# Kernel tuning notes

Measured on AMD Instinct MI355X. Metric: run time of the kernel, lower is better.

The kernel has to match this reference:

```python
import jax, jax.numpy as jnp
import numpy as np

B, N, C, F = 8, 3, 64, 128
H = W = 128


def _up2(x):
    # nearest-neighbor upsample by 2 on the last two axes
    return jnp.repeat(jnp.repeat(x, 2, axis=-2), 2, axis=-1)


def setup_inputs() -> dict:
    key = jax.random.key(0)
    ks = jax.random.split(key, 12)
    s = lambda k, shp, fan: jax.random.normal(k, shp, jnp.float32) * (1.0 / np.sqrt(fan))
    return {
        "contexts": jax.random.normal(ks[0], (B, N, C, H, W), jnp.float32),
        "mainstream": jax.random.normal(ks[1], (B, F, H // 2, W // 2), jnp.float32),
        "Wc": s(ks[2], (C, C), C),        # W_context 1x1 conv weight [out,in]
        "bc": jnp.zeros((C,), jnp.float32),
        "Wf": s(ks[3], (C, F), F),        # W_feat 1x1
        "bf": jnp.zeros((C,), jnp.float32),
        "Wk": s(ks[4], (C, F), F),        # W_key_feat 1x1
        "bk": jnp.zeros((C,), jnp.float32),
        "Vw": s(ks[5], (C, F, 3, 3), F * 9),  # values_conv 3x3, OIHW
        "Vb": jnp.zeros((C,), jnp.float32),
    }


def reference(contexts, mainstream, Wc, bc, Wf, bf, Wk, bk, Vw, Vb):
    # contexts: [B,N,C,H,W], mainstream: [B,F,h,w]
    bias = lambda b: b[None, :, None, None]
    queries = jnp.einsum('bfhw,cf->bchw', mainstream, Wf) + bias(bf)       # [B,C,h,w]
    keys_m = jnp.einsum('bfhw,cf->bchw', mainstream, Wk) + bias(bk)        # [B,C,h,w]
    values = jax.lax.conv_general_dilated(
        mainstream, Vw, (1, 1), 'SAME',
        dimension_numbers=('NCHW', 'OIHW', 'NCHW')) + bias(Vb)             # [B,C,h,w]

    # stack contexts with upsampled mainstream keys, project with W_context (1x1)
    keys_stack = jnp.concatenate([contexts, _up2(keys_m)[:, None]], axis=1)  # [B,N+1,C,H,W]
    keys_proj = jnp.einsum('bnchw,dc->bndhw', keys_stack, Wc) + bc[None, None, :, None, None]

    q_up = _up2(queries)                                                    # [B,C,H,W]
    logits = jnp.einsum('bnchw,bchw->bnhw', keys_proj, q_up)                # [B,N+1,H,W]
    attn = jax.nn.softmax(logits, axis=1)                                   # softmax over contexts

    vals_stack = jnp.concatenate([contexts, _up2(values)[:, None]], axis=1) # [B,N+1,C,H,W]
    out = jnp.einsum('bnchw,bnhw->bchw', vals_stack, attn)                  # [B,C,H,W]
    return out
```

## Files before the change

### kernel.cpp

```cpp
#include <hip/hip_runtime.h>
#include <math.h>

#define CH   64
#define FD   128
#define HS   64
#define FS   128
#define NB   8
#define NCTX 3

#define WS_BQ   4227072
#define WS_AVH  4227136
#define WS_AQH  4264000
#define WS_AQL  4268096
#define WS_AKH  4272192
#define WS_AKL  4276288

typedef short  s16x8  __attribute__((ext_vector_type(8)));
typedef float  f32x16 __attribute__((ext_vector_type(16)));

__device__ inline unsigned short bf16_rne(float x) {
  unsigned u = __float_as_uint(x);
  u += 0x7FFFu + ((u >> 16) & 1u);
  return (unsigned short)(u >> 16);
}
__device__ inline void split2(float x, unsigned short& h, unsigned short& l) {
  h = bf16_rne(x);
  l = bf16_rne(x - __uint_as_float((unsigned)h << 16));
}

__global__ __launch_bounds__(256) void afrag_prep(
    const float* __restrict__ Wc, const float* __restrict__ Wf,
    const float* __restrict__ bf, const float* __restrict__ Wk,
    const float* __restrict__ Vw, float* __restrict__ ws) {
  int id = blockIdx.x * 256 + threadIdx.x;
  unsigned short* avh = (unsigned short*)(ws + WS_AVH);
  unsigned short* aqh = (unsigned short*)(ws + WS_AQH);
  unsigned short* aql = (unsigned short*)(ws + WS_AQL);
  unsigned short* akh = (unsigned short*)(ws + WS_AKH);
  unsigned short* akl = (unsigned short*)(ws + WS_AKL);

  if (id < 9216) {
    int tile = id / 4608, rem = id % 4608;
    int q = rem >> 6, l = rem & 63;
    int am = l & 31, kh = l >> 5;
    int c = tile * 32 + am, tap = q >> 3, kf = q & 7;
#pragma unroll
    for (int j = 0; j < 8; ++j) {
      int f = kf * 16 + kh * 8 + j;
      avh[id * 8 + j] = bf16_rne(Vw[(c * FD + f) * 9 + tap]);
    }
  } else if (id < 10240) {
    int i2 = id - 9216;
    int tile = i2 >> 9, rem = i2 & 511;
    int q = rem >> 6, l = rem & 63;
    int am = l & 31, kh = l >> 5;
    int c = tile * 32 + am;
#pragma unroll
    for (int j = 0; j < 8; ++j) {
      int f = q * 16 + kh * 8 + j;
      float acc = 0.f;
      for (int d = 0; d < CH; ++d)
        acc = fmaf(Wc[d * CH + c], Wf[d * FD + f], acc);
      unsigned short h, lo; split2(acc, h, lo);
      aqh[i2 * 8 + j] = h; aql[i2 * 8 + j] = lo;
    }
  } else if (id < 11264) {
    int i3 = id - 10240;
    int tile = i3 >> 9, rem = i3 & 511;
    int q = rem >> 6, l = rem & 63;
    int am = l & 31, kh = l >> 5;
    int c = tile * 32 + am;
#pragma unroll
    for (int j = 0; j < 8; ++j) {
      int f = q * 16 + kh * 8 + j;
      unsigned short h, lo; split2(Wk[c * FD + f], h, lo);
      akh[i3 * 8 + j] = h; akl[i3 * 8 + j] = lo;
    }
  } else if (id < 11328) {
    int c = id - 11264;
    float acc = 0.f;
    for (int d = 0; d < CH; ++d) acc = fmaf(Wc[d * CH + c], bf[d], acc);
    ws[WS_BQ + c] = acc;
  }
}

__global__ __launch_bounds__(512) void fused_kernel(
    const float* __restrict__ m, const float* __restrict__ Vb,
    const float* __restrict__ bk, const float* __restrict__ ctx,
    float* __restrict__ out, const float* __restrict__ ws) {
  const int b = blockIdx.x >> 6, y = blockIdx.x & 63;
  const int t = threadIdx.x, lane = t & 63;
  const int wave = __builtin_amdgcn_readfirstlane(t >> 6);
  const int am = lane & 31, kh = lane >> 5;

  __shared__ __align__(16) union {
    short HI[3][8][66][2][8];
    struct {
      float  QT[CH * HS];
      float  VAL[CH * HS];
      float4 wpart[2][4][3][16];
      float  L3row[HS];
    } p;
  } U;
  __shared__ float l3red[2][64];

  if (t < 96) {
    int row = t / 32, kf = (t >> 2) & 7, khh = (t >> 1) & 1, col = (t & 1) * 65;
    s16x8 z;
#pragma unroll
    for (int j = 0; j < 8; ++j) z[j] = 0;
    *(s16x8*)&U.HI[row][kf][col][khh][0] = z;
  }

#pragma unroll
  for (int i = 0; i < 6; ++i) {
    const int tk = wave * 6 + i;
    const int row = tk >> 4, kf = (tk >> 1) & 7, khh = tk & 1;
    const int yy = y + row - 1;
    s16x8 hi;
    if (yy >= 0 && yy < HS) {
#pragma unroll
      for (int j = 0; j < 8; ++j) {
        const int f = kf * 16 + khh * 8 + j;
        hi[j] = (short)bf16_rne(m[((b * FD + f) * HS + yy) * HS + lane]);
      }
    } else {
#pragma unroll
      for (int j = 0; j < 8; ++j) hi[j] = 0;
    }
    *(s16x8*)&U.HI[row][kf][lane + 1][khh][0] = hi;
  }
  __syncthreads();

  const int ct = (wave >> 1) & 1;
  const int xh = wave & 1;
  const int x0 = xh * 32, ch0 = ct * 32;

  f32x16 acc, q1, q2, k1, k2;
  float l3part = 0.f;

  if (wave < 4) {
    const unsigned short* avh = (const unsigned short*)(ws + WS_AVH);
#pragma unroll
    for (int i = 0; i < 16; ++i) acc[i] = 0.f;
#pragma unroll 8
    for (int q = 0; q < 72; ++q) {
      const int tap = q >> 3, kf = q & 7;
      const s16x8 ah = *(const s16x8*)(avh + ((ct * 72 + q) * 64 + lane) * 8);
      const s16x8 bh = *(const s16x8*)&U.HI[tap / 3][kf][x0 + am + tap % 3][kh][0];
      acc = __builtin_amdgcn_mfma_f32_32x32x16_bf16(ah, bh, acc, 0, 0, 0);
    }
  } else {
    const unsigned short* aqh = (const unsigned short*)(ws + WS_AQH);
    const unsigned short* aql = (const unsigned short*)(ws + WS_AQL);
    const unsigned short* akh = (const unsigned short*)(ws + WS_AKH);
    const unsigned short* akl = (const unsigned short*)(ws + WS_AKL);
#pragma unroll
    for (int i = 0; i < 16; ++i) { q1[i] = 0.f; q2[i] = 0.f; k1[i] = 0.f; k2[i] = 0.f; }
#pragma unroll
    for (int q = 0; q < 8; ++q) {
      const s16x8 bh = *(const s16x8*)&U.HI[1][q][x0 + am + 1][kh][0];
      s16x8 bl;
#pragma unroll
      for (int j = 0; j < 8; ++j) {
        const float mv = m[((b * FD + q * 16 + kh * 8 + j) * HS + y) * HS + x0 + am];
        const float hf = __uint_as_float(((unsigned)(unsigned short)bh[j]) << 16);
        bl[j] = (short)bf16_rne(mv - hf);
      }
      const s16x8 ah = *(const s16x8*)(aqh + ((ct * 8 + q) * 64 + lane) * 8);
      const s16x8 al = *(const s16x8*)(aql + ((ct * 8 + q) * 64 + lane) * 8);
      const s16x8 kah = *(const s16x8*)(akh + ((ct * 8 + q) * 64 + lane) * 8);
      const s16x8 kal = *(const s16x8*)(akl + ((ct * 8 + q) * 64 + lane) * 8);
      q1 = __builtin_amdgcn_mfma_f32_32x32x16_bf16(ah, bh, q1, 0, 0, 0);
      q1 = __builtin_amdgcn_mfma_f32_32x32x16_bf16(al, bh, q1, 0, 0, 0);
      q2 = __builtin_amdgcn_mfma_f32_32x32x16_bf16(ah, bl, q2, 0, 0, 0);
      k1 = __builtin_amdgcn_mfma_f32_32x32x16_bf16(kah, bh, k1, 0, 0, 0);
      k1 = __builtin_amdgcn_mfma_f32_32x32x16_bf16(kal, bh, k1, 0, 0, 0);
      k2 = __builtin_amdgcn_mfma_f32_32x32x16_bf16(kah, bl, k2, 0, 0, 0);
    }
  }
  __syncthreads();

  if (wave < 4) {
#pragma unroll
    for (int r = 0; r < 16; ++r) {
      const int c = ch0 + (r & 3) + 8 * (r >> 2) + 4 * kh;
      U.p.VAL[c * HS + x0 + am] = acc[r] + Vb[c];
    }
  } else {
#pragma unroll
    for (int r = 0; r < 16; ++r) {
      const int c = ch0 + (r & 3) + 8 * (r >> 2) + 4 * kh;
      const float qvv = q1[r] + q2[r] + ws[WS_BQ + c];
      const float kvv = k1[r] + k2[r] + bk[c];
      U.p.QT[c * HS + x0 + am] = qvv;
      l3part = fmaf(qvv, kvv, l3part);
    }
    if (ct == 1) l3red[xh][lane] = l3part;
  }
  __syncthreads();

  if (wave == 4 || wave == 5) {
    float s = l3part + l3red[xh][lane];
    s += __shfl_xor(s, 32, 64);
    if (kh == 0) U.p.L3row[x0 + am] = s;
  }
  __syncthreads();

  const int u    = t >> 8;
  const int tt   = t & 255;
  const int quad = tt & 15;
  const int cg   = tt >> 4;
  const int wv   = tt >> 6;
  const int c0   = cg * 4;
  const int hrow = 2 * y + u;
  const int cs = FS * FS, ns = CH * FS * FS;

  float* op = out + (size_t)(b * CH) * FS * FS + (size_t)hrow * FS;
  const float* cb = ctx + (size_t)(b * NCTX * CH) * cs + (size_t)hrow * FS;

#pragma unroll 1
  for (int x2 = 0; x2 < 2; ++x2) {
    const int x = x2 * 64 + quad * 4;
    const int w2 = x >> 1;

    float4 cv[3][4];
    float2 qv[4];
#pragma unroll
    for (int j = 0; j < 4; ++j) {
      const int c = c0 + j;
      cv[0][j] = *(const float4*)(cb + x + c * cs);
      cv[1][j] = *(const float4*)(cb + x + ns + c * cs);
      cv[2][j] = *(const float4*)(cb + x + 2 * ns + c * cs);
      qv[j] = *(const float2*)&U.p.QT[c * HS + w2];
    }

    float4 pl[3];
#pragma unroll
    for (int n = 0; n < 3; ++n) {
      pl[n].x = pl[n].y = pl[n].z = pl[n].w = 0.f;
#pragma unroll
      for (int j = 0; j < 4; ++j) {
        pl[n].x = fmaf(cv[n][j].x, qv[j].x, pl[n].x);
        pl[n].y = fmaf(cv[n][j].y, qv[j].x, pl[n].y);
        pl[n].z = fmaf(cv[n][j].z, qv[j].y, pl[n].z);
        pl[n].w = fmaf(cv[n][j].w, qv[j].y, pl[n].w);
      }
    }

#pragma unroll
    for (int n = 0; n < 3; ++n) {
      pl[n].x += __shfl_xor(pl[n].x, 16, 64);
      pl[n].y += __shfl_xor(pl[n].y, 16, 64);
      pl[n].z += __shfl_xor(pl[n].z, 16, 64);
      pl[n].w += __shfl_xor(pl[n].w, 16, 64);
      pl[n].x += __shfl_xor(pl[n].x, 32, 64);
      pl[n].y += __shfl_xor(pl[n].y, 32, 64);
      pl[n].z += __shfl_xor(pl[n].z, 32, 64);
      pl[n].w += __shfl_xor(pl[n].w, 32, 64);
    }
    __syncthreads();
    if ((lane >> 4) == 0) {
#pragma unroll
      for (int n = 0; n < 3; ++n) U.p.wpart[u][wv][n][quad] = pl[n];
    }
    __syncthreads();

    float4 L[3];
#pragma unroll
    for (int n = 0; n < 3; ++n) {
      const float4 p0 = U.p.wpart[u][0][n][quad];
      const float4 p1 = U.p.wpart[u][1][n][quad];
      const float4 p2 = U.p.wpart[u][2][n][quad];
      const float4 p3 = U.p.wpart[u][3][n][quad];
      L[n].x = (p0.x + p1.x) + (p2.x + p3.x);
      L[n].y = (p0.y + p1.y) + (p2.y + p3.y);
      L[n].z = (p0.z + p1.z) + (p2.z + p3.z);
      L[n].w = (p0.w + p1.w) + (p2.w + p3.w);
    }
    const float2 l3v = *(const float2*)&U.p.L3row[w2];

    float A0[4], A1[4], A2[4], A3[4];
    const float* L0p = (const float*)&L[0];
    const float* L1p = (const float*)&L[1];
    const float* L2p = (const float*)&L[2];
#pragma unroll
    for (int k = 0; k < 4; ++k) {
      float L0 = L0p[k], L1 = L1p[k], L2 = L2p[k];
      float L3 = (k < 2) ? l3v.x : l3v.y;
      float mx = fmaxf(fmaxf(L0, L1), fmaxf(L2, L3));
      float e0 = __expf(L0 - mx), e1 = __expf(L1 - mx);
      float e2 = __expf(L2 - mx), e3 = __expf(L3 - mx);
      float inv = 1.f / (e0 + e1 + e2 + e3);
      A0[k] = e0 * inv; A1[k] = e1 * inv; A2[k] = e2 * inv; A3[k] = e3 * inv;
    }

#pragma unroll
    for (int j = 0; j < 4; ++j) {
      const int c = c0 + j;
      const float2 vv = *(const float2*)&U.p.VAL[c * HS + w2];
      float4 o;
      o.x = fmaf(A0[0], cv[0][j].x, fmaf(A1[0], cv[1][j].x, fmaf(A2[0], cv[2][j].x, A3[0] * vv.x)));
      o.y = fmaf(A0[1], cv[0][j].y, fmaf(A1[1], cv[1][j].y, fmaf(A2[1], cv[2][j].y, A3[1] * vv.x)));
      o.z = fmaf(A0[2], cv[0][j].z, fmaf(A1[2], cv[1][j].z, fmaf(A2[2], cv[2][j].z, A3[2] * vv.y)));
      o.w = fmaf(A0[3], cv[0][j].w, fmaf(A1[3], cv[1][j].w, fmaf(A2[3], cv[2][j].w, A3[3] * vv.y)));
      *(float4*)(op + x + c * cs) = o;
    }
  }
}

extern "C" void kernel_launch(void* const* d_in, const int* in_sizes, int n_in,
                              void* d_out, int out_size, void* d_ws, size_t ws_size,
                              hipStream_t stream) {
  const float* ctx = (const float*)d_in[0];
  const float* ms  = (const float*)d_in[1];
  const float* Wc  = (const float*)d_in[2];
  const float* Wf  = (const float*)d_in[4];
  const float* bf  = (const float*)d_in[5];
  const float* Wk  = (const float*)d_in[6];
  const float* bk  = (const float*)d_in[7];
  const float* Vw  = (const float*)d_in[8];
  const float* Vb  = (const float*)d_in[9];
  float* ws  = (float*)d_ws;
  float* out = (float*)d_out;

  afrag_prep<<<45, 256, 0, stream>>>(Wc, Wf, bf, Wk, Vw, ws);
  fused_kernel<<<NB * HS, 512, 0, stream>>>(ms, Vb, bk, ctx, out, ws);
}
```

Baseline: 244.9 us.

## Split each row block into two half-width blocks of 256 threads

The fused kernel now launches twice as many blocks, each handling half the 64-wide mainstream row (32 columns plus halo) with 256 threads instead of 512. Each block builds a smaller bf16 tile, runs one value-conv wave pair and one query/key wave pair, and loops over the two upsampled output rows instead of two x halves. Query/value fragments are hoisted out of that loop, and the L3 reduction is folded directly into register reads, which removes one barrier. The goal is more blocks for better CU occupancy and load balance on the memory-bound context streaming, at the cost of redundant halo loads of the mainstream input.

```diff
diff --git a/kernel.cpp b/kernel.cpp
--- a/kernel.cpp
+++ b/kernel.cpp
@@ -84,62 +84,56 @@
   }
 }
 
-__global__ __launch_bounds__(512) void fused_kernel(
+__global__ __launch_bounds__(256) void fused_kernel(
     const float* __restrict__ m, const float* __restrict__ Vb,
     const float* __restrict__ bk, const float* __restrict__ ctx,
     float* __restrict__ out, const float* __restrict__ ws) {
-  const int b = blockIdx.x >> 6, y = blockIdx.x & 63;
+  const int b  = blockIdx.x >> 7;
+  const int y  = (blockIdx.x >> 1) & 63;
+  const int xh = blockIdx.x & 1;
   const int t = threadIdx.x, lane = t & 63;
   const int wave = __builtin_amdgcn_readfirstlane(t >> 6);
   const int am = lane & 31, kh = lane >> 5;
 
   __shared__ __align__(16) union {
-    short HI[3][8][66][2][8];
+    short HI[3][8][34][2][8];
     struct {
-      float  QT[CH * HS];
-      float  VAL[CH * HS];
-      float4 wpart[2][4][3][16];
-      float  L3row[HS];
+      float  QT[CH][34];
+      float  VAL[CH][34];
+      float4 wpart[4][3][16];
+      float  l3red[2][64];
     } p;
   } U;
-  __shared__ float l3red[2][64];
-
-  if (t < 96) {
-    int row = t / 32, kf = (t >> 2) & 7, khh = (t >> 1) & 1, col = (t & 1) * 65;
-    s16x8 z;
-#pragma unroll
-    for (int j = 0; j < 8; ++j) z[j] = 0;
-    *(s16x8*)&U.HI[row][kf][col][khh][0] = z;
-  }
-
-#pragma unroll
-  for (int i = 0; i < 6; ++i) {
-    const int tk = wave * 6 + i;
+
+  const int gx0 = 32 * xh - 1;
+#pragma unroll
+  for (int i = 0; i < 12; ++i) {
+    const int tk = wave * 12 + i;
     const int row = tk >> 4, kf = (tk >> 1) & 7, khh = tk & 1;
     const int yy = y + row - 1;
-    s16x8 hi;
-    if (yy >= 0 && yy < HS) {
-#pragma unroll
-      for (int j = 0; j < 8; ++j) {
-        const int f = kf * 16 + khh * 8 + j;
-        hi[j] = (short)bf16_rne(m[((b * FD + f) * HS + yy) * HS + lane]);
+    const int gx = gx0 + lane;
+    if (lane < 34) {
+      s16x8 hi;
+      if (yy >= 0 && yy < HS && gx >= 0 && gx < HS) {
+#pragma unroll
+        for (int j = 0; j < 8; ++j) {
+          const int f = kf * 16 + khh * 8 + j;
+          hi[j] = (short)bf16_rne(m[((b * FD + f) * HS + yy) * HS + gx]);
+        }
+      } else {
+#pragma unroll
+        for (int j = 0; j < 8; ++j) hi[j] = 0;
       }
-    } else {
-#pragma unroll
-      for (int j = 0; j < 8; ++j) hi[j] = 0;
-    }
-    *(s16x8*)&U.HI[row][kf][lane + 1][khh][0] = hi;
+      *(s16x8*)&U.HI[row][kf][lane][khh][0] = hi;
+    }
   }
   __syncthreads();
 
-  const int ct = (wave >> 1) & 1;
-  const int xh = wave & 1;
-  const int x0 = xh * 32, ch0 = ct * 32;
-
+  const int ct = wave & 1;
   f32x16 acc, q1, q2, k1, k2;
   float l3part = 0.f;
 
-  if (wave < 4) {
+  if (wave < 2) {
     const unsigned short* avh = (const unsigned short*)(ws + WS_AVH);
 #pragma unroll
     for (int i = 0; i < 16; ++i) acc[i] = 0.f;
@@ -147,7 +141,7 @@
     for (int q = 0; q < 72; ++q) {
       const int tap = q >> 3, kf = q & 7;
       const s16x8 ah = *(const s16x8*)(avh + ((ct * 72 + q) * 64 + lane) * 8);
-      const s16x8 bh = *(const s16x8*)&U.HI[tap / 3][kf][x0 + am + tap % 3][kh][0];
+      const s16x8 bh = *(const s16x8*)&U.HI[tap / 3][kf][am + tap % 3][kh][0];
       acc = __builtin_amdgcn_mfma_f32_32x32x16_bf16(ah, bh, acc, 0, 0, 0);
     }
   } else {
@@ -159,11 +153,11 @@
     for (int i = 0; i < 16; ++i) { q1[i] = 0.f; q2[i] = 0.f; k1[i] = 0.f; k2[i] = 0.f; }
 #pragma unroll
     for (int q = 0; q < 8; ++q) {
-      const s16x8 bh = *(const s16x8*)&U.HI[1][q][x0 + am + 1][kh][0];
+      const s16x8 bh = *(const s16x8*)&U.HI[1][q][am + 1][kh][0];
       s16x8 bl;
 #pragma unroll
       for (int j = 0; j < 8; ++j) {
-        const float mv = m[((b * FD + q * 16 + kh * 8 + j) * HS + y) * HS + x0 + am];
+        const float mv = m[((b * FD + q * 16 + kh * 8 + j) * HS + y) * HS + 32 * xh + am];
         const float hf = __uint_as_float(((unsigned)(unsigned short)bh[j]) << 16);
         bl[j] = (short)bf16_rne(mv - hf);
       }
@@ -181,58 +175,57 @@
   }
   __syncthreads();
 
-  if (wave < 4) {
+  if (wave < 2) {
 #pragma unroll
     for (int r = 0; r < 16; ++r) {
-      const int c = ch0 + (r & 3) + 8 * (r >> 2) + 4 * kh;
-      U.p.VAL[c * HS + x0 + am] = acc[r] + Vb[c];
+      const int c = ct * 32 + (r & 3) + 8 * (r >> 2) + 4 * kh;
+      U.p.VAL[c][am] = acc[r] + Vb[c];
     }
   } else {
 #pragma unroll
     for (int r = 0; r < 16; ++r) {
-      const int c = ch0 + (r & 3) + 8 * (r >> 2) + 4 * kh;
+      const int c = ct * 32 + (r & 3) + 8 * (r >> 2) + 4 * kh;
       const float qvv = q1[r] + q2[r] + ws[WS_BQ + c];
       const float kvv = k1[r] + k2[r] + bk[c];
-      U.p.QT[c * HS + x0 + am] = qvv;
+      U.p.QT[c][am] = qvv;
       l3part = fmaf(qvv, kvv, l3part);
     }
-    if (ct == 1) l3red[xh][lane] = l3part;
+    U.p.l3red[ct][lane] = l3part;
   }
   __syncthreads();
 
-  if (wave == 4 || wave == 5) {
-    float s = l3part + l3red[xh][lane];
-    s += __shfl_xor(s, 32, 64);
-    if (kh == 0) U.p.L3row[x0 + am] = s;
-  }
-  __syncthreads();
-
-  const int u    = t >> 8;
-  const int tt   = t & 255;
-  const int quad = tt & 15;
-  const int cg   = tt >> 4;
-  const int wv   = tt >> 6;
+  const int quad = t & 15;
+  const int cg   = t >> 4;
   const int c0   = cg * 4;
-  const int hrow = 2 * y + u;
+  const int x    = 64 * xh + quad * 4;
+  const int hx   = quad * 2;
   const int cs = FS * FS, ns = CH * FS * FS;
 
-  float* op = out + (size_t)(b * CH) * FS * FS + (size_t)hrow * FS;
-  const float* cb = ctx + (size_t)(b * NCTX * CH) * cs + (size_t)hrow * FS;
+  const float l3a = U.p.l3red[0][hx]     + U.p.l3red[0][hx + 32]
+                  + U.p.l3red[1][hx]     + U.p.l3red[1][hx + 32];
+  const float l3b = U.p.l3red[0][hx + 1] + U.p.l3red[0][hx + 33]
+                  + U.p.l3red[1][hx + 1] + U.p.l3red[1][hx + 33];
+
+  float2 qv[4], vv[4];
+#pragma unroll
+  for (int j = 0; j < 4; ++j) {
+    qv[j] = *(const float2*)&U.p.QT[c0 + j][hx];
+    vv[j] = *(const float2*)&U.p.VAL[c0 + j][hx];
+  }
 
 #pragma unroll 1
-  for (int x2 = 0; x2 < 2; ++x2) {
-    const int x = x2 * 64 + quad * 4;
-    const int w2 = x >> 1;
+  for (int u = 0; u < 2; ++u) {
+    const int hrow = 2 * y + u;
+    const float* cb = ctx + (size_t)(b * NCTX * CH) * cs + (size_t)hrow * FS + x;
+    float* op = out + (size_t)(b * CH) * cs + (size_t)hrow * FS + x;
 
     float4 cv[3][4];
-    float2 qv[4];
 #pragma unroll
     for (int j = 0; j < 4; ++j) {
       const int c = c0 + j;
-      cv[0][j] = *(const float4*)(cb + x + c * cs);
-      cv[1][j] = *(const float4*)(cb + x + ns + c * cs);
-      cv[2][j] = *(const float4*)(cb + x + 2 * ns + c * cs);
-      qv[j] = *(const float2*)&U.p.QT[c * HS + w2];
+      cv[0][j] = *(const float4*)(cb + c * cs);
+      cv[1][j] = *(const float4*)(cb + ns + c * cs);
+      cv[2][j] = *(const float4*)(cb + 2 * ns + c * cs);
     }
 
     float4 pl[3];
@@ -262,23 +255,22 @@
     __syncthreads();
     if ((lane >> 4) == 0) {
 #pragma unroll
-      for (int n = 0; n < 3; ++n) U.p.wpart[u][wv][n][quad] = pl[n];
+      for (int n = 0; n < 3; ++n) U.p.wpart[wave][n][quad] = pl[n];
     }
     __syncthreads();
 
     float4 L[3];
 #pragma unroll
     for (int n = 0; n < 3; ++n) {
-      const float4 p0 = U.p.wpart[u][0][n][quad];
-      const float4 p1 = U.p.wpart[u][1][n][quad];
-      const float4 p2 = U.p.wpart[u][2][n][quad];
-      const float4 p3 = U.p.wpart[u][3][n][quad];
+      const float4 p0 = U.p.wpart[0][n][quad];
+      const float4 p1 = U.p.wpart[1][n][quad];
+      const float4 p2 = U.p.wpart[2][n][quad];
+      const float4 p3 = U.p.wpart[3][n][quad];
       L[n].x = (p0.x + p1.x) + (p2.x + p3.x);
       L[n].y = (p0.y + p1.y) + (p2.y + p3.y);
       L[n].z = (p0.z + p1.z) + (p2.z + p3.z);
       L[n].w = (p0.w + p1.w) + (p2.w + p3.w);
     }
-    const float2 l3v = *(const float2*)&U.p.L3row[w2];
 
     float A0[4], A1[4], A2[4], A3[4];
     const float* L0p = (const float*)&L[0];
@@ -287,7 +279,7 @@
 #pragma unroll
     for (int k = 0; k < 4; ++k) {
       float L0 = L0p[k], L1 = L1p[k], L2 = L2p[k];
-      float L3 = (k < 2) ? l3v.x : l3v.y;
+      float L3 = (k < 2) ? l3a : l3b;
       float mx = fmaxf(fmaxf(L0, L1), fmaxf(L2, L3));
       float e0 = __expf(L0 - mx), e1 = __expf(L1 - mx);
       float e2 = __expf(L2 - mx), e3 = __expf(L3 - mx);
@@ -298,13 +290,12 @@
 #pragma unroll
     for (int j = 0; j < 4; ++j) {
       const int c = c0 + j;
-      const float2 vv = *(const float2*)&U.p.VAL[c * HS + w2];
       float4 o;
-      o.x = fmaf(A0[0], cv[0][j].x, fmaf(A1[0], cv[1][j].x, fmaf(A2[0], cv[2][j].x, A3[0] * vv.x)));
-      o.y = fmaf(A0[1], cv[0][j].y, fmaf(A1[1], cv[1][j].y, fmaf(A2[1], cv[2][j].y, A3[1] * vv.x)));
-      o.z = fmaf(A0[2], cv[0][j].z, fmaf(A1[2], cv[1][j].z, fmaf(A2[2], cv[2][j].z, A3[2] * vv.y)));
-      o.w = fmaf(A0[3], cv[0][j].w, fmaf(A1[3], cv[1][j].w, fmaf(A2[3], cv[2][j].w, A3[3] * vv.y)));
-      *(float4*)(op + x + c * cs) = o;
+      o.x = fmaf(A0[0], cv[0][j].x, fmaf(A1[0], cv[1][j].x, fmaf(A2[0], cv[2][j].x, A3[0] * vv[j].x)));
+      o.y = fmaf(A0[1], cv[0][j].y, fmaf(A1[1], cv[1][j].y, fmaf(A2[1], cv[2][j].y, A3[1] * vv[j].x)));
+      o.z = fmaf(A0[2], cv[0][j].z, fmaf(A1[2], cv[1][j].z, fmaf(A2[2], cv[2][j].z, A3[2] * vv[j].y)));
+      o.w = fmaf(A0[3], cv[0][j].w, fmaf(A1[3], cv[1][j].w, fmaf(A2[3], cv[2][j].w, A3[3] * vv[j].y)));
+      *(float4*)(op + c * cs) = o;
     }
   }
 }
@@ -325,5 +316,5 @@
   float* out = (float*)d_out;
 
   afrag_prep<<<45, 256, 0, stream>>>(Wc, Wf, bf, Wk, Vw, ws);
-  fused_kernel<<<NB * HS, 512, 0, stream>>>(ms, Vb, bk, ctx, out, ws);
-}
+  fused_kernel<<<NB * HS * 2, 256, 0, stream>>>(ms, Vb, bk, ctx, out, ws);
+}
```

Measured after the change: 258.7 us. 1.06x slower.

## Double-buffer context rows into LDS via async global-to-LDS loads

Applied to the files above, without the earlier changes.

Context activations now arrive through async global_load_lds copies into a double-buffered shared-memory tile. Wave 0 issues each copy, and the first copy starts while the MFMA projection phase is still running. The output phase is restructured so all 512 threads handle one 64-pixel half-row unit at a time, across four units. This lets the next unit's loads overlap with the current unit's softmax and stores. In exchange, the kernel uses about 98KB of extra LDS, which likely drops occupancy to one block per CU. It also makes a single wave issue all the context loads and uses hand-placed waitcnt barriers.

```diff
diff --git a/kernel.cpp b/kernel.cpp
--- a/kernel.cpp
+++ b/kernel.cpp
@@ -17,6 +17,8 @@
 
 typedef short  s16x8  __attribute__((ext_vector_type(8)));
 typedef float  f32x16 __attribute__((ext_vector_type(16)));
+typedef __attribute__((address_space(3))) unsigned int lds_u32;
+typedef __attribute__((address_space(1))) const unsigned int glob_u32;
 
 __device__ inline unsigned short bf16_rne(float x) {
   unsigned u = __float_as_uint(x);
@@ -26,6 +28,12 @@
 __device__ inline void split2(float x, unsigned short& h, unsigned short& l) {
   h = bf16_rne(x);
   l = bf16_rne(x - __uint_as_float((unsigned)h << 16));
+}
+
+__device__ inline void rbar() {
+  asm volatile("s_waitcnt lgkmcnt(0)" ::: "memory");
+  __builtin_amdgcn_s_barrier();
+  __builtin_amdgcn_sched_barrier(0);
 }
 
 __global__ __launch_bounds__(256) void afrag_prep(
@@ -84,6 +92,19 @@
   }
 }
 
+__device__ inline void issue_unit(const float* __restrict__ ctx, float* slot,
+                                  int b, int hrow, int x0, int lane) {
+  const int rl = lane >> 4;
+  const int pxl = (lane & 15) * 4;
+#pragma unroll
+  for (int i = 0; i < 48; ++i) {
+    const int r = i * 4 + rl;
+    const int n = r >> 6, c = r & 63;
+    const float* g = ctx + ((((size_t)b * NCTX + n) * CH + c) * FS + hrow) * FS + x0 + pxl;
+    __builtin_amdgcn_global_load_lds((glob_u32*)g, (lds_u32*)(slot + i * 256), 16, 0, 0);
+  }
+}
+
 __global__ __launch_bounds__(512) void fused_kernel(
     const float* __restrict__ m, const float* __restrict__ Vb,
     const float* __restrict__ bk, const float* __restrict__ ctx,
@@ -96,12 +117,13 @@
   __shared__ __align__(16) union {
     short HI[3][8][66][2][8];
     struct {
-      float  QT[CH * HS];
-      float  VAL[CH * HS];
-      float4 wpart[2][4][3][16];
-      float  L3row[HS];
+      float  QT[CH][64];
+      float  VAL[CH][64];
+      float4 wpart[8][3][16];
+      float  L3[64];
     } p;
   } U;
+  __shared__ __align__(16) float CTXB[2][NCTX][CH][64];
   __shared__ float l3red[2][64];
 
   if (t < 96) {
@@ -130,7 +152,10 @@
     }
     *(s16x8*)&U.HI[row][kf][lane + 1][khh][0] = hi;
   }
-  __syncthreads();
+
+  __builtin_amdgcn_sched_barrier(0);
+  if (wave == 0) issue_unit(ctx, &CTXB[0][0][0][0], b, 2 * y, 0, lane);
+  rbar();
 
   const int ct = (wave >> 1) & 1;
   const int xh = wave & 1;
@@ -179,13 +204,13 @@
       k2 = __builtin_amdgcn_mfma_f32_32x32x16_bf16(kah, bl, k2, 0, 0, 0);
     }
   }
-  __syncthreads();
+  rbar();
 
   if (wave < 4) {
 #pragma unroll
     for (int r = 0; r < 16; ++r) {
       const int c = ch0 + (r & 3) + 8 * (r >> 2) + 4 * kh;
-      U.p.VAL[c * HS + x0 + am] = acc[r] + Vb[c];
+      U.p.VAL[c][x0 + am] = acc[r] + Vb[c];
     }
   } else {
 #pragma unroll
@@ -193,63 +218,57 @@
       const int c = ch0 + (r & 3) + 8 * (r >> 2) + 4 * kh;
       const float qvv = q1[r] + q2[r] + ws[WS_BQ + c];
       const float kvv = k1[r] + k2[r] + bk[c];
-      U.p.QT[c * HS + x0 + am] = qvv;
+      U.p.QT[c][x0 + am] = qvv;
       l3part = fmaf(qvv, kvv, l3part);
     }
     if (ct == 1) l3red[xh][lane] = l3part;
   }
-  __syncthreads();
+  rbar();
 
   if (wave == 4 || wave == 5) {
     float s = l3part + l3red[xh][lane];
     s += __shfl_xor(s, 32, 64);
-    if (kh == 0) U.p.L3row[x0 + am] = s;
-  }
-  __syncthreads();
-
-  const int u    = t >> 8;
-  const int tt   = t & 255;
-  const int quad = tt & 15;
-  const int cg   = tt >> 4;
-  const int wv   = tt >> 6;
-  const int c0   = cg * 4;
-  const int hrow = 2 * y + u;
-  const int cs = FS * FS, ns = CH * FS * FS;
-
-  float* op = out + (size_t)(b * CH) * FS * FS + (size_t)hrow * FS;
-  const float* cb = ctx + (size_t)(b * NCTX * CH) * cs + (size_t)hrow * FS;
+    if (kh == 0) U.p.L3[x0 + am] = s;
+  }
+
+  if (wave == 0) asm volatile("s_waitcnt vmcnt(0)" ::: "memory");
+  rbar();
+
+  const int quad = lane & 15;
+  const int cg   = t >> 4;
+  const int c0   = 2 * cg;
+  const int cs = FS * FS;
 
 #pragma unroll 1
-  for (int x2 = 0; x2 < 2; ++x2) {
-    const int x = x2 * 64 + quad * 4;
-    const int w2 = x >> 1;
-
-    float4 cv[3][4];
-    float2 qv[4];
-#pragma unroll
-    for (int j = 0; j < 4; ++j) {
-      const int c = c0 + j;
-      cv[0][j] = *(const float4*)(cb + x + c * cs);
-      cv[1][j] = *(const float4*)(cb + x + ns + c * cs);
-      cv[2][j] = *(const float4*)(cb + x + 2 * ns + c * cs);
-      qv[j] = *(const float2*)&U.p.QT[c * HS + w2];
+  for (int k = 0; k < 4; ++k) {
+    if (wave == 0 && k < 3) {
+      const int kn = k + 1;
+      issue_unit(ctx, &CTXB[kn & 1][0][0][0], b, 2 * y + (kn >> 1), 64 * (kn & 1), lane);
+    }
+    const float* CB = &CTXB[k & 1][0][0][0];
+    const int x2 = k & 1, u = k >> 1;
+    const int hrow = 2 * y + u;
+    const int x = 64 * x2 + quad * 4;
+    const int hx = 32 * x2 + quad * 2;
+
+    float4 cv[3][2];
+    float2 qv[2], vv[2];
+#pragma unroll
+    for (int j = 0; j < 2; ++j) {
+      qv[j] = *(const float2*)&U.p.QT[c0 + j][hx];
+      vv[j] = *(const float2*)&U.p.VAL[c0 + j][hx];
+#pragma unroll
+      for (int n = 0; n < 3; ++n)
+        cv[n][j] = *(const float4*)(CB + ((n * CH + c0 + j) * 64 + quad * 4));
     }
 
     float4 pl[3];
 #pragma unroll
     for (int n = 0; n < 3; ++n) {
-      pl[n].x = pl[n].y = pl[n].z = pl[n].w = 0.f;
-#pragma unroll
-      for (int j = 0; j < 4; ++j) {
-        pl[n].x = fmaf(cv[n][j].x, qv[j].x, pl[n].x);
-        pl[n].y = fmaf(cv[n][j].y, qv[j].x, pl[n].y);
-        pl[n].z = fmaf(cv[n][j].z, qv[j].y, pl[n].z);
-        pl[n].w = fmaf(cv[n][j].w, qv[j].y, pl[n].w);
-      }
-    }
-
-#pragma unroll
-    for (int n = 0; n < 3; ++n) {
+      pl[n].x = fmaf(cv[n][1].x, qv[1].x, cv[n][0].x * qv[0].x);
+      pl[n].y = fmaf(cv[n][1].y, qv[1].x, cv[n][0].y * qv[0].x);
+      pl[n].z = fmaf(cv[n][1].z, qv[1].y, cv[n][0].z * qv[0].y);
+      pl[n].w = fmaf(cv[n][1].w, qv[1].y, cv[n][0].w * qv[0].y);
       pl[n].x += __shfl_xor(pl[n].x, 16, 64);
       pl[n].y += __shfl_xor(pl[n].y, 16, 64);
       pl[n].z += __shfl_xor(pl[n].z, 16, 64);
@@ -259,52 +278,55 @@
       pl[n].z += __shfl_xor(pl[n].z, 32, 64);
       pl[n].w += __shfl_xor(pl[n].w, 32, 64);
     }
-    __syncthreads();
     if ((lane >> 4) == 0) {
 #pragma unroll
-      for (int n = 0; n < 3; ++n) U.p.wpart[u][wv][n][quad] = pl[n];
-    }
-    __syncthreads();
+      for (int n = 0; n < 3; ++n) U.p.wpart[wave][n][quad] = pl[n];
+    }
+    rbar();
 
     float4 L[3];
 #pragma unroll
     for (int n = 0; n < 3; ++n) {
-      const float4 p0 = U.p.wpart[u][0][n][quad];
-      const float4 p1 = U.p.wpart[u][1][n][quad];
-      const float4 p2 = U.p.wpart[u][2][n][quad];
-      const float4 p3 = U.p.wpart[u][3][n][quad];
-      L[n].x = (p0.x + p1.x) + (p2.x + p3.x);
-      L[n].y = (p0.y + p1.y) + (p2.y + p3.y);
-      L[n].z = (p0.z + p1.z) + (p2.z + p3.z);
-      L[n].w = (p0.w + p1.w) + (p2.w + p3.w);
-    }
-    const float2 l3v = *(const float2*)&U.p.L3row[w2];
+      float4 s = U.p.wpart[0][n][quad];
+#pragma unroll
+      for (int w = 1; w < 8; ++w) {
+        const float4 p = U.p.wpart[w][n][quad];
+        s.x += p.x; s.y += p.y; s.z += p.z; s.w += p.w;
+      }
+      L[n] = s;
+    }
+    const float l3a = U.p.L3[hx], l3b = U.p.L3[hx + 1];
 
     float A0[4], A1[4], A2[4], A3[4];
     const float* L0p = (const float*)&L[0];
     const float* L1p = (const float*)&L[1];
     const float* L2p = (const float*)&L[2];
 #pragma unroll
-    for (int k = 0; k < 4; ++k) {
-      float L0 = L0p[k], L1 = L1p[k], L2 = L2p[k];
-      float L3 = (k < 2) ? l3v.x : l3v.y;
-      float mx = fmaxf(fmaxf(L0, L1), fmaxf(L2, L3));
+    for (int kk = 0; kk < 4; ++kk) {
+      float L0 = L0p[kk], L1 = L1p[kk], L2 = L2p[kk];
+      float L3v = (kk < 2) ? l3a : l3b;
+      float mx = fmaxf(fmaxf(L0, L1), fmaxf(L2, L3v));
       float e0 = __expf(L0 - mx), e1 = __expf(L1 - mx);
-      float e2 = __expf(L2 - mx), e3 = __expf(L3 - mx);
+      float e2 = __expf(L2 - mx), e3 = __expf(L3v - mx);
       float inv = 1.f / (e0 + e1 + e2 + e3);
-      A0[k] = e0 * inv; A1[k] = e1 * inv; A2[k] = e2 * inv; A3[k] = e3 * inv;
-    }
-
-#pragma unroll
-    for (int j = 0; j < 4; ++j) {
+      A0[kk] = e0 * inv; A1[kk] = e1 * inv; A2[kk] = e2 * inv; A3[kk] = e3 * inv;
+    }
+
+    float* op = out + (size_t)(b * CH) * cs + (size_t)hrow * FS + x;
+#pragma unroll
+    for (int j = 0; j < 2; ++j) {
       const int c = c0 + j;
-      const float2 vv = *(const float2*)&U.p.VAL[c * HS + w2];
       float4 o;
-      o.x = fmaf(A0[0], cv[0][j].x, fmaf(A1[0], cv[1][j].x, fmaf(A2[0], cv[2][j].x, A3[0] * vv.x)));
-      o.y = fmaf(A0[1], cv[0][j].y, fmaf(A1[1], cv[1][j].y, fmaf(A2[1], cv[2][j].y, A3[1] * vv.x)));
-      o.z = fmaf(A0[2], cv[0][j].z, fmaf(A1[2], cv[1][j].z, fmaf(A2[2], cv[2][j].z, A3[2] * vv.y)));
-      o.w = fmaf(A0[3], cv[0][j].w, fmaf(A1[3], cv[1][j].w, fmaf(A2[3], cv[2][j].w, A3[3] * vv.y)));
-      *(float4*)(op + x + c * cs) = o;
+      o.x = fmaf(A0[0], cv[0][j].x, fmaf(A1[0], cv[1][j].x, fmaf(A2[0], cv[2][j].x, A3[0] * vv[j].x)));
+      o.y = fmaf(A0[1], cv[0][j].y, fmaf(A1[1], cv[1][j].y, fmaf(A2[1], cv[2][j].y, A3[1] * vv[j].x)));
+      o.z = fmaf(A0[2], cv[0][j].z, fmaf(A1[2], cv[1][j].z, fmaf(A2[2], cv[2][j].z, A3[2] * vv[j].y)));
+      o.w = fmaf(A0[3], cv[0][j].w, fmaf(A1[3], cv[1][j].w, fmaf(A2[3], cv[2][j].w, A3[3] * vv[j].y)));
+      *(float4*)(op + c * cs) = o;
+    }
+
+    if (k < 3) {
+      if (wave == 0) asm volatile("s_waitcnt vmcnt(2)" ::: "memory");
+      rbar();
     }
   }
 }
```

After: 254.4 us. +3.9%, slower.

## Remap attention phase so channel reduction stays within a wave, dropping block barriers

Applied to the files above, without the earlier changes.

Reassigns threads in the attention/output phase so each 16-lane group holds all 64 channels for 4 pixels. The channel-dot reduction then finishes with intra-16-lane shuffles instead of a cross-wave LDS reduction guarded by two __syncthreads per iteration. QT/VAL are padded to 65 columns to ease LDS bank conflicts, and launch bounds now request 4 blocks per SM. The trade-off is less coalesced global access: each 16-lane group touches 64 channel planes with only 16-byte contiguity per lane, and the tighter register budget could cause spills.

```diff
diff --git a/kernel.cpp b/kernel.cpp
--- a/kernel.cpp
+++ b/kernel.cpp
@@ -84,7 +84,7 @@
   }
 }
 
-__global__ __launch_bounds__(512) void fused_kernel(
+__global__ __launch_bounds__(512, 4) void fused_kernel(
     const float* __restrict__ m, const float* __restrict__ Vb,
     const float* __restrict__ bk, const float* __restrict__ ctx,
     float* __restrict__ out, const float* __restrict__ ws) {
@@ -96,10 +96,9 @@
   __shared__ __align__(16) union {
     short HI[3][8][66][2][8];
     struct {
-      float  QT[CH * HS];
-      float  VAL[CH * HS];
-      float4 wpart[2][4][3][16];
-      float  L3row[HS];
+      float  QT[CH][65];
+      float  VAL[CH][65];
+      float  L3[64];
     } p;
   } U;
   __shared__ float l3red[2][64];
@@ -185,7 +184,7 @@
 #pragma unroll
     for (int r = 0; r < 16; ++r) {
       const int c = ch0 + (r & 3) + 8 * (r >> 2) + 4 * kh;
-      U.p.VAL[c * HS + x0 + am] = acc[r] + Vb[c];
+      U.p.VAL[c][x0 + am] = acc[r] + Vb[c];
     }
   } else {
 #pragma unroll
@@ -193,7 +192,7 @@
       const int c = ch0 + (r & 3) + 8 * (r >> 2) + 4 * kh;
       const float qvv = q1[r] + q2[r] + ws[WS_BQ + c];
       const float kvv = k1[r] + k2[r] + bk[c];
-      U.p.QT[c * HS + x0 + am] = qvv;
+      U.p.QT[c][x0 + am] = qvv;
       l3part = fmaf(qvv, kvv, l3part);
     }
     if (ct == 1) l3red[xh][lane] = l3part;
@@ -203,36 +202,34 @@
   if (wave == 4 || wave == 5) {
     float s = l3part + l3red[xh][lane];
     s += __shfl_xor(s, 32, 64);
-    if (kh == 0) U.p.L3row[x0 + am] = s;
+    if (kh == 0) U.p.L3[x0 + am] = s;
   }
   __syncthreads();
 
-  const int u    = t >> 8;
-  const int tt   = t & 255;
-  const int quad = tt & 15;
-  const int cg   = tt >> 4;
-  const int wv   = tt >> 6;
-  const int c0   = cg * 4;
+  const int cl = lane & 15;
+  const int pp = lane >> 4;
+  const int u  = wave & 1;
+  const int xq = wave >> 1;
   const int hrow = 2 * y + u;
-  const int cs = FS * FS, ns = CH * FS * FS;
-
-  float* op = out + (size_t)(b * CH) * FS * FS + (size_t)hrow * FS;
-  const float* cb = ctx + (size_t)(b * NCTX * CH) * cs + (size_t)hrow * FS;
+  const int cs = FS * FS;
+  const float* cbase = ctx + (size_t)(b * NCTX * CH) * cs + (size_t)hrow * FS;
+  float* obase = out + (size_t)(b * CH) * cs + (size_t)hrow * FS;
 
 #pragma unroll 1
-  for (int x2 = 0; x2 < 2; ++x2) {
-    const int x = x2 * 64 + quad * 4;
-    const int w2 = x >> 1;
+  for (int j = 0; j < 2; ++j) {
+    const int px0 = xq * 32 + j * 16 + pp * 4;
+    const int hx0 = px0 >> 1;
 
     float4 cv[3][4];
-    float2 qv[4];
-#pragma unroll
-    for (int j = 0; j < 4; ++j) {
-      const int c = c0 + j;
-      cv[0][j] = *(const float4*)(cb + x + c * cs);
-      cv[1][j] = *(const float4*)(cb + x + ns + c * cs);
-      cv[2][j] = *(const float4*)(cb + x + 2 * ns + c * cs);
-      qv[j] = *(const float2*)&U.p.QT[c * HS + w2];
+    float2 qv[4], vv[4];
+#pragma unroll
+    for (int i = 0; i < 4; ++i) {
+      const int c = 4 * cl + i;
+      qv[i] = *(const float2*)&U.p.QT[c][hx0];
+      vv[i] = *(const float2*)&U.p.VAL[c][hx0];
+#pragma unroll
+      for (int n = 0; n < 3; ++n)
+        cv[n][i] = *(const float4*)(cbase + (n * CH + c) * cs + px0);
     }
 
     float4 pl[3];
@@ -240,71 +237,49 @@
     for (int n = 0; n < 3; ++n) {
       pl[n].x = pl[n].y = pl[n].z = pl[n].w = 0.f;
 #pragma unroll
-      for (int j = 0; j < 4; ++j) {
-        pl[n].x = fmaf(cv[n][j].x, qv[j].x, pl[n].x);
-        pl[n].y = fmaf(cv[n][j].y, qv[j].x, pl[n].y);
-        pl[n].z = fmaf(cv[n][j].z, qv[j].y, pl[n].z);
-        pl[n].w = fmaf(cv[n][j].w, qv[j].y, pl[n].w);
+      for (int i = 0; i < 4; ++i) {
+        pl[n].x = fmaf(cv[n][i].x, qv[i].x, pl[n].x);
+        pl[n].y = fmaf(cv[n][i].y, qv[i].x, pl[n].y);
+        pl[n].z = fmaf(cv[n][i].z, qv[i].y, pl[n].z);
+        pl[n].w = fmaf(cv[n][i].w, qv[i].y, pl[n].w);
       }
     }
-
-#pragma unroll
-    for (int n = 0; n < 3; ++n) {
-      pl[n].x += __shfl_xor(pl[n].x, 16, 64);
-      pl[n].y += __shfl_xor(pl[n].y, 16, 64);
-      pl[n].z += __shfl_xor(pl[n].z, 16, 64);
-      pl[n].w += __shfl_xor(pl[n].w, 16, 64);
-      pl[n].x += __shfl_xor(pl[n].x, 32, 64);
-      pl[n].y += __shfl_xor(pl[n].y, 32, 64);
-      pl[n].z += __shfl_xor(pl[n].z, 32, 64);
-      pl[n].w += __shfl_xor(pl[n].w, 32, 64);
-    }
-    __syncthreads();
-    if ((lane >> 4) == 0) {
-#pragma unroll
-      for (int n = 0; n < 3; ++n) U.p.wpart[u][wv][n][quad] = pl[n];
-    }
-    __syncthreads();
-
-    float4 L[3];
-#pragma unroll
-    for (int n = 0; n < 3; ++n) {
-      const float4 p0 = U.p.wpart[u][0][n][quad];
-      const float4 p1 = U.p.wpart[u][1][n][quad];
-      const float4 p2 = U.p.wpart[u][2][n][quad];
-      const float4 p3 = U.p.wpart[u][3][n][quad];
-      L[n].x = (p0.x + p1.x) + (p2.x + p3.x);
-      L[n].y = (p0.y + p1.y) + (p2.y + p3.y);
-      L[n].z = (p0.z + p1.z) + (p2.z + p3.z);
-      L[n].w = (p0.w + p1.w) + (p2.w + p3.w);
-    }
-    const float2 l3v = *(const float2*)&U.p.L3row[w2];
+#pragma unroll
+    for (int mk = 1; mk <= 8; mk <<= 1) {
+#pragma unroll
+      for (int n = 0; n < 3; ++n) {
+        pl[n].x += __shfl_xor(pl[n].x, mk, 16);
+        pl[n].y += __shfl_xor(pl[n].y, mk, 16);
+        pl[n].z += __shfl_xor(pl[n].z, mk, 16);
+        pl[n].w += __shfl_xor(pl[n].w, mk, 16);
+      }
+    }
+    const float l3a = U.p.L3[hx0], l3b = U.p.L3[hx0 + 1];
 
     float A0[4], A1[4], A2[4], A3[4];
-    const float* L0p = (const float*)&L[0];
-    const float* L1p = (const float*)&L[1];
-    const float* L2p = (const float*)&L[2];
+    const float* L0p = (const float*)&pl[0];
+    const float* L1p = (const float*)&pl[1];
+    const float* L2p = (const float*)&pl[2];
 #pragma unroll
     for (int k = 0; k < 4; ++k) {
       float L0 = L0p[k], L1 = L1p[k], L2 = L2p[k];
-      float L3 = (k < 2) ? l3v.x : l3v.y;
-      float mx = fmaxf(fmaxf(L0, L1), fmaxf(L2, L3));
+      float L3v = (k < 2) ? l3a : l3b;
+      float mx = fmaxf(fmaxf(L0, L1), fmaxf(L2, L3v));
       float e0 = __expf(L0 - mx), e1 = __expf(L1 - mx);
-      float e2 = __expf(L2 - mx), e3 = __expf(L3 - mx);
+      float e2 = __expf(L2 - mx), e3 = __expf(L3v - mx);
       float inv = 1.f / (e0 + e1 + e2 + e3);
       A0[k] = e0 * inv; A1[k] = e1 * inv; A2[k] = e2 * inv; A3[k] = e3 * inv;
     }
 
 #pragma unroll
-    for (int j = 0; j < 4; ++j) {
-      const int c = c0 + j;
-      const float2 vv = *(const float2*)&U.p.VAL[c * HS + w2];
+    for (int i = 0; i < 4; ++i) {
+      const int c = 4 * cl + i;
       float4 o;
-      o.x = fmaf(A0[0], cv[0][j].x, fmaf(A1[0], cv[1][j].x, fmaf(A2[0], cv[2][j].x, A3[0] * vv.x)));
-      o.y = fmaf(A0[1], cv[0][j].y, fmaf(A1[1], cv[1][j].y, fmaf(A2[1], cv[2][j].y, A3[1] * vv.x)));
-      o.z = fmaf(A0[2], cv[0][j].z, fmaf(A1[2], cv[1][j].z, fmaf(A2[2], cv[2][j].z, A3[2] * vv.y)));
-      o.w = fmaf(A0[3], cv[0][j].w, fmaf(A1[3], cv[1][j].w, fmaf(A2[3], cv[2][j].w, A3[3] * vv.y)));
-      *(float4*)(op + x + c * cs) = o;
+      o.x = fmaf(A0[0], cv[0][i].x, fmaf(A1[0], cv[1][i].x, fmaf(A2[0], cv[2][i].x, A3[0] * vv[i].x)));
+      o.y = fmaf(A0[1], cv[0][i].y, fmaf(A1[1], cv[1][i].y, fmaf(A2[1], cv[2][i].y, A3[1] * vv[i].x)));
+      o.z = fmaf(A0[2], cv[0][i].z, fmaf(A1[2], cv[1][i].z, fmaf(A2[2], cv[2][i].z, A3[2] * vv[i].y)));
+      o.w = fmaf(A0[3], cv[0][i].w, fmaf(A1[3], cv[1][i].w, fmaf(A2[3], cv[2][i].w, A3[3] * vv[i].y)));
+      *(float4*)(obase + c * cs + px0) = o;
     }
   }
 }
```

New measurement: 254.6 us. 4.0% more time.
